# Kernel optimization log

Measured on AMD Instinct MI355X. Metric: run time of the kernel, lower is better.

The kernel has to match this reference:

```python
import jax, jax.numpy as jnp
import numpy as np

N_NODES = 50000
N_EDGES = 800000
N_GRAPHS = 64
IN_C, HID_C, OUT_C = 768, 128, 1


def setup_inputs() -> dict:
    key = jax.random.key(0)
    ks = jax.random.split(key, 9)
    x = jax.random.normal(ks[0], (N_NODES, IN_C), dtype=jnp.float32)
    edge_index = jax.random.randint(ks[1], (2, N_EDGES), 0, N_NODES, dtype=jnp.int32)
    batch = jnp.sort(jax.random.randint(ks[2], (N_NODES,), 0, N_GRAPHS, dtype=jnp.int32))
    s1 = 1.0 / np.sqrt(IN_C)
    s2 = 1.0 / np.sqrt(HID_C)
    W1 = jax.random.normal(ks[3], (IN_C, HID_C), dtype=jnp.float32) * s1
    b1 = jnp.zeros((HID_C,), dtype=jnp.float32)
    W2 = jax.random.normal(ks[4], (HID_C, HID_C), dtype=jnp.float32) * s2
    b2 = jnp.zeros((HID_C,), dtype=jnp.float32)
    Wl = jax.random.normal(ks[5], (HID_C, OUT_C), dtype=jnp.float32) * s2
    bl = jnp.zeros((OUT_C,), dtype=jnp.float32)
    return {"x": x, "edge_index": edge_index, "batch": batch,
            "W1": W1, "b1": b1, "W2": W2, "b2": b2, "Wl": Wl, "bl": bl}


def gcn_conv(x, W, b, src, dst, n_nodes):
    """PyG GCNConv: linear transform, symmetric norm with self-loops, scatter-add."""
    xl = x @ W  # [N, C_out]
    # in-degree including self-loop
    deg = jax.ops.segment_sum(jnp.ones_like(dst, dtype=xl.dtype), dst,
                              num_segments=n_nodes) + 1.0
    dinv = jax.lax.rsqrt(deg)  # deg >= 1 so safe
    norm = dinv[src] * dinv[dst]  # [E]
    agg = jax.ops.segment_sum(norm[:, None] * xl[src], dst, num_segments=n_nodes)
    # self-loop message: dinv[i]^2 * xl[i]
    agg = agg + xl * (dinv * dinv)[:, None]
    return agg + b


def reference(x, edge_index, batch, W1, b1, W2, b2, Wl, bl):
    src, dst = edge_index[0], edge_index[1]
    n = x.shape[0]
    h = jax.nn.relu(gcn_conv(x, W1, b1, src, dst, n))
    # dropout is identity in eval mode
    h = jax.nn.relu(gcn_conv(h, W2, b2, src, dst, n))
    # global mean pool over graphs
    sums = jax.ops.segment_sum(h, batch, num_segments=N_GRAPHS)
    cnts = jax.ops.segment_sum(jnp.ones((n,), dtype=h.dtype), batch,
                               num_segments=N_GRAPHS)
    pooled = sums / jnp.maximum(cnts, 1.0)[:, None]
    return pooled @ Wl + bl
```

## Files before the change

kernel.cpp:

```cpp
#include <hip/hip_runtime.h>

#define N_NODES  50000
#define N_EDGES  800000
#define N_GRAPHS 64
#define N_CHUNK  4
#define ZREP     16
#define SCAN_BLOCKS 196
#define GATHER_BLOCKS 1568

typedef unsigned short u16x8 __attribute__((ext_vector_type(8)));
typedef short s16x8 __attribute__((ext_vector_type(8)));
typedef float f32x4 __attribute__((ext_vector_type(4)));

__device__ __forceinline__ float bf2f(unsigned short h) {
    return __uint_as_float((unsigned)h << 16);
}
__device__ __forceinline__ unsigned short f2bf(float f) {
    unsigned u = __float_as_uint(f);
    unsigned r = (u + 0x7FFFu + ((u >> 16) & 1u)) >> 16;
    return (unsigned short)r;
}
__device__ __forceinline__ unsigned pk2(float a, float b) {
    return (unsigned)f2bf(a) | ((unsigned)f2bf(b) << 16);
}


__global__ void zero_int_kernel(int* __restrict__ p, int n) {
    for (int i = blockIdx.x * blockDim.x + threadIdx.x; i < n; i += gridDim.x * blockDim.x)
        p[i] = 0;
}

__global__ void hist_kernel(const int* __restrict__ ei, int* __restrict__ cnt) {
    const int* dst = ei + N_EDGES;
    for (int e = blockIdx.x * blockDim.x + threadIdx.x; e < N_EDGES; e += gridDim.x * blockDim.x)
        atomicAdd(&cnt[dst[e]], 1);
}

__global__ void scanA_kernel(const int* __restrict__ cnt, int* __restrict__ bsum,
                             float* __restrict__ dinv) {
    __shared__ int wsum[4];
    int t = threadIdx.x;
    int i = blockIdx.x * 256 + t;
    int v = cnt[i];
    if (i < N_NODES) dinv[i] = rsqrtf((float)v + 1.f);
    int s = v;
    #pragma unroll
    for (int off = 1; off < 64; off <<= 1) s += __shfl_xor(s, off);
    if ((t & 63) == 0) wsum[t >> 6] = s;
    __syncthreads();
    if (t == 0) bsum[blockIdx.x] = wsum[0] + wsum[1] + wsum[2] + wsum[3];
}

__global__ void scanB_kernel(const int* __restrict__ bsum, int* __restrict__ boff) {
    __shared__ int wsum[4];
    int t = threadIdx.x;
    int lane = t & 63, w = t >> 6;
    int v = (t < SCAN_BLOCKS) ? bsum[t] : 0;
    int s = v;
    #pragma unroll
    for (int off = 1; off < 64; off <<= 1) {
        int u = __shfl_up(s, off);
        if (lane >= off) s += u;
    }
    if (lane == 63) wsum[w] = s;
    __syncthreads();
    int wo = 0;
    for (int j = 0; j < w; ++j) wo += wsum[j];
    if (t < SCAN_BLOCKS) boff[t] = wo + s - v;
}

__global__ void scanC_kernel(int* __restrict__ cnt, const int* __restrict__ boff,
                             int* __restrict__ rowptr) {
    __shared__ int wsum[4];
    int t = threadIdx.x;
    int i = blockIdx.x * 256 + t;
    int lane = t & 63, w = t >> 6;
    int v = cnt[i];
    int s = v;
    #pragma unroll
    for (int off = 1; off < 64; off <<= 1) {
        int u = __shfl_up(s, off);
        if (lane >= off) s += u;
    }
    if (lane == 63) wsum[w] = s;
    __syncthreads();
    int wo = 0;
    for (int j = 0; j < w; ++j) wo += wsum[j];
    rowptr[i] = boff[blockIdx.x] + wo + s - v;
    cnt[i] = 0;
}

__global__ void fill_kernel(const int* __restrict__ ei, const int* __restrict__ rowptr,
                            int* __restrict__ fill, const float* __restrict__ dinv,
                            int2* __restrict__ csr) {
    const int* src = ei;
    const int* dst = ei + N_EDGES;
    for (int e = blockIdx.x * blockDim.x + threadIdx.x; e < N_EDGES; e += gridDim.x * blockDim.x) {
        int s = src[e], d = dst[e];
        int pos = rowptr[d] + atomicAdd(&fill[d], 1);
        csr[pos] = make_int2(s, __float_as_int(dinv[s] * dinv[d]));
    }
}

__global__ void gcount_bs_kernel(const int* __restrict__ batch, float* __restrict__ cntg,
                                 float* __restrict__ zsumR) {
    int g = threadIdx.x;
    if (g >= N_GRAPHS) return;
    #pragma unroll
    for (int r = 0; r < ZREP; ++r) zsumR[r * N_GRAPHS + g] = 0.f;
    int lo = 0, hi = N_NODES;
    while (lo < hi) { int mid = (lo + hi) >> 1; if (batch[mid] < g) lo = mid + 1; else hi = mid; }
    int a = lo;
    lo = 0; hi = N_NODES;
    while (lo < hi) { int mid = (lo + hi) >> 1; if (batch[mid] < g + 1) lo = mid + 1; else hi = mid; }
    cntg[g] = (float)(lo - a);
}

__global__ void prep_w_kernel(const float* __restrict__ W1, const float* __restrict__ W2,
                              unsigned short* __restrict__ w1h, unsigned short* __restrict__ w1l,
                              unsigned short* __restrict__ w2h, unsigned short* __restrict__ w2l) {
    const int n1 = 768 * 128, n2 = 128 * 128;
    for (int i = blockIdx.x * blockDim.x + threadIdx.x; i < n1 + n2; i += gridDim.x * blockDim.x) {
        if (i < n1) {
            int k = i >> 7, c = i & 127;
            float w = W1[i];
            unsigned short hi = f2bf(w);
            unsigned short lo = f2bf(w - bf2f(hi));
            w1h[c * 768 + k] = hi;
            w1l[c * 768 + k] = lo;
        } else {
            int j = i - n1;
            int k = j >> 7, c = j & 127;
            float w = W2[j];
            unsigned short hi = f2bf(w);
            unsigned short lo = f2bf(w - bf2f(hi));
            w2h[c * 128 + k] = hi;
            w2l[c * 128 + k] = lo;
        }
    }
}

template<int K, bool BF16A>
__global__ __launch_bounds__(256) void gemm_mfma(const void* __restrict__ Av,
                                                 const unsigned short* __restrict__ Wth,
                                                 const unsigned short* __restrict__ Wtl,
                                                 unsigned short* __restrict__ C, int M) {
    __shared__ unsigned short Xs[128 * 40];
    __shared__ unsigned short Wh[128 * 40];
    __shared__ unsigned short Wl[128 * 40];

    const int tid  = threadIdx.x;
    const int row0 = blockIdx.x * 128;
    const int trow  = tid >> 1;
    const int thalf = (tid & 1) * 16;

    int grow = row0 + trow;
    if (grow >= M) grow = M - 1;
    const float* xpf = (const float*)Av + (long)grow * K + thalf;
    const unsigned short* xpb = (const unsigned short*)Av + (long)grow * K + thalf;
    const unsigned short* wph = Wth + (long)trow * K + thalf;
    const unsigned short* wpl = Wtl + (long)trow * K + thalf;

    f32x4 acc[8][2];
    #pragma unroll
    for (int rf = 0; rf < 8; ++rf)
        #pragma unroll
        for (int cf = 0; cf < 2; ++cf)
            acc[rf][cf] = (f32x4){0.f, 0.f, 0.f, 0.f};

    float4 f0, f1, f2, f3;
    uint4 b0, b1;
    if constexpr (!BF16A) {
        f0 = *(const float4*)(xpf);
        f1 = *(const float4*)(xpf + 4);
        f2 = *(const float4*)(xpf + 8);
        f3 = *(const float4*)(xpf + 12);
    } else {
        b0 = *(const uint4*)(xpb);
        b1 = *(const uint4*)(xpb + 8);
    }

    const int l   = tid & 63;
    const int wv  = tid >> 6;
    const int lr  = l & 15;
    const int lk8 = (l >> 4) * 8;

    for (int k0 = 0; k0 < K; k0 += 32) {
        uint4 wh0 = ((const uint4*)(wph + k0))[0];
        uint4 wh1 = ((const uint4*)(wph + k0))[1];
        uint4 wl0 = ((const uint4*)(wpl + k0))[0];
        uint4 wl1 = ((const uint4*)(wpl + k0))[1];
        unsigned short* xrow = &Xs[trow * 40 + thalf];
        if constexpr (!BF16A) {
            *(uint4*)(xrow)     = make_uint4(pk2(f0.x, f0.y), pk2(f0.z, f0.w), pk2(f1.x, f1.y), pk2(f1.z, f1.w));
            *(uint4*)(xrow + 8) = make_uint4(pk2(f2.x, f2.y), pk2(f2.z, f2.w), pk2(f3.x, f3.y), pk2(f3.z, f3.w));
        } else {
            *(uint4*)(xrow)     = b0;
            *(uint4*)(xrow + 8) = b1;
        }
        *(uint4*)&Wh[trow * 40 + thalf]     = wh0;
        *(uint4*)&Wh[trow * 40 + thalf + 8] = wh1;
        *(uint4*)&Wl[trow * 40 + thalf]     = wl0;
        *(uint4*)&Wl[trow * 40 + thalf + 8] = wl1;
        __syncthreads();

        if (k0 + 32 < K) {
            if constexpr (!BF16A) {
                f0 = *(const float4*)(xpf + k0 + 32);
                f1 = *(const float4*)(xpf + k0 + 36);
                f2 = *(const float4*)(xpf + k0 + 40);
                f3 = *(const float4*)(xpf + k0 + 44);
            } else {
                b0 = *(const uint4*)(xpb + k0 + 32);
                b1 = *(const uint4*)(xpb + k0 + 40);
            }
        }

        s16x8 xb[8], whf[2], wlf[2];
        #pragma unroll
        for (int rf = 0; rf < 8; ++rf)
            xb[rf] = *(const s16x8*)&Xs[(rf * 16 + lr) * 40 + lk8];
        #pragma unroll
        for (int cf = 0; cf < 2; ++cf) {
            whf[cf] = *(const s16x8*)&Wh[(wv * 32 + cf * 16 + lr) * 40 + lk8];
            wlf[cf] = *(const s16x8*)&Wl[(wv * 32 + cf * 16 + lr) * 40 + lk8];
        }
        #pragma unroll
        for (int rf = 0; rf < 8; ++rf)
            #pragma unroll
            for (int cf = 0; cf < 2; ++cf) {
                acc[rf][cf] = __builtin_amdgcn_mfma_f32_16x16x32_bf16(wlf[cf], xb[rf], acc[rf][cf], 0, 0, 0);
                acc[rf][cf] = __builtin_amdgcn_mfma_f32_16x16x32_bf16(whf[cf], xb[rf], acc[rf][cf], 0, 0, 0);
            }
        __syncthreads();
    }

    const int c4 = (l >> 4) * 4;
    #pragma unroll
    for (int rf = 0; rf < 8; ++rf) {
        int r = row0 + rf * 16 + lr;
        if (r < M) {
            #pragma unroll
            for (int cf = 0; cf < 2; ++cf) {
                int cb = wv * 32 + cf * 16 + c4;
                ushort4 v;
                v.x = f2bf(acc[rf][cf][0]);
                v.y = f2bf(acc[rf][cf][1]);
                v.z = f2bf(acc[rf][cf][2]);
                v.w = f2bf(acc[rf][cf][3]);
                *(ushort4*)(C + ((long)(cb >> 5) * N_NODES + r) * 32 + (cb & 31)) = v;
            }
        }
    }
}

template<int MODE>
__global__ __launch_bounds__(256, 6) void gather_all_kernel(
        const unsigned short* __restrict__ xlc, const float* __restrict__ dinv,
        const int* __restrict__ rowptr, const int2* __restrict__ csr,
        const float* __restrict__ bias, unsigned short* __restrict__ outbuf,
        const float* __restrict__ Wl, const int* __restrict__ batch,
        float* __restrict__ zsumR) {
    const int lane = threadIdx.x & 63;
    const int half = lane & 1;
    const int c0   = half * 16;

    const int grp   = blockIdx.x & 7;
    const int chunk = grp & 3;
    const unsigned short* xc = xlc + (long)chunk * N_NODES * 32;

    const int cblk = (blockIdx.x >> 3) + (grp >> 2) * 196;
    const int wvc  = cblk * 4 + (threadIdx.x >> 6);
    const int slot = wvc * 32 + (lane >> 1);
    const bool vn  = slot < N_NODES;
    const int node = vn ? slot : N_NODES - 1;

    const int start = rowptr[node];
    const int end   = vn ? rowptr[node + 1] : start;
    const float di  = dinv[node];

    const u16x8* srow = (const u16x8*)(xc + (long)node * 32 + c0);
    u16x8 s0 = srow[0], s1 = srow[1];

    float acc[16];
    #pragma unroll
    for (int j = 0; j < 16; ++j) acc[j] = 0.f;

    int e = start;
    for (; e + 1 < end; e += 2) {
        int2 cA = csr[e];
        int2 cB = csr[e + 1];
        float wA = __int_as_float(cA.y);
        float wB = __int_as_float(cB.y);
        const u16x8* rA = (const u16x8*)(xc + (long)cA.x * 32 + c0);
        const u16x8* rB = (const u16x8*)(xc + (long)cB.x * 32 + c0);
        u16x8 a0 = rA[0], a1 = rA[1];
        u16x8 b0 = rB[0], b1 = rB[1];
        #pragma unroll
        for (int j = 0; j < 8; ++j) {
            acc[j]     = fmaf(wA, bf2f(a0[j]), acc[j]);
            acc[j + 8] = fmaf(wA, bf2f(a1[j]), acc[j + 8]);
        }
        #pragma unroll
        for (int j = 0; j < 8; ++j) {
            acc[j]     = fmaf(wB, bf2f(b0[j]), acc[j]);
            acc[j + 8] = fmaf(wB, bf2f(b1[j]), acc[j + 8]);
        }
    }
    if (e < end) {
        int2 cA = csr[e];
        float wA = __int_as_float(cA.y);
        const u16x8* rA = (const u16x8*)(xc + (long)cA.x * 32 + c0);
        u16x8 a0 = rA[0], a1 = rA[1];
        #pragma unroll
        for (int j = 0; j < 8; ++j) {
            acc[j]     = fmaf(wA, bf2f(a0[j]), acc[j]);
            acc[j + 8] = fmaf(wA, bf2f(a1[j]), acc[j + 8]);
        }
    }

    const float w2 = di * di;
    const float* bch = bias + chunk * 32 + c0;
    float s[16];
    #pragma unroll
    for (int j = 0; j < 8; ++j) {
        s[j]     = fmaxf(fmaf(w2, bf2f(s0[j]), acc[j])     + bch[j],     0.f);
        s[j + 8] = fmaxf(fmaf(w2, bf2f(s1[j]), acc[j + 8]) + bch[j + 8], 0.f);
    }

    if (MODE == 0) {
        if (vn) {
            unsigned short* op = outbuf + (long)node * 128 + chunk * 32 + c0;
            u16x8 o0, o1;
            #pragma unroll
            for (int j = 0; j < 8; ++j) {
                o0[j] = f2bf(s[j]);
                o1[j] = f2bf(s[j + 8]);
            }
            ((u16x8*)op)[0] = o0;
            ((u16x8*)op)[1] = o1;
        }
    } else {
        const float* wch = Wl + chunk * 32 + c0;
        float z = 0.f;
        #pragma unroll
        for (int j = 0; j < 16; ++j) z = fmaf(s[j], wch[j], z);
        z += __shfl_xor(z, 1);
        if (!vn || half) z = 0.f;
        int b = batch[node];
        int b0v = __shfl(b, 0);
        bool uniform = __all(b == b0v);
        if (uniform) {
            #pragma unroll
            for (int off = 1; off < 64; off <<= 1) z += __shfl_xor(z, off);
            if (lane == 0)
                atomicAdd(&zsumR[(blockIdx.x & (ZREP - 1)) * N_GRAPHS + b0v], z);
        } else if (vn && !half) {
            atomicAdd(&zsumR[((lane >> 1) & (ZREP - 1)) * N_GRAPHS + b], z);
        }
    }
}

__global__ void out_kernel(const float* __restrict__ zsumR, const float* __restrict__ cntg,
                           const float* __restrict__ bl, float* __restrict__ out) {
    int g = threadIdx.x;
    if (g < N_GRAPHS) {
        float z = 0.f;
        #pragma unroll
        for (int r = 0; r < ZREP; ++r) z += zsumR[r * N_GRAPHS + g];
        out[g] = z / fmaxf(cntg[g], 1.f) + bl[0];
    }
}


extern "C" void kernel_launch(void* const* d_in, const int* in_sizes, int n_in,
                              void* d_out, int out_size, void* d_ws, size_t ws_size,
                              hipStream_t stream) {
    const float* x    = (const float*)d_in[0];
    const int*   ei   = (const int*)d_in[1];
    const int*   batch= (const int*)d_in[2];
    const float* W1   = (const float*)d_in[3];
    const float* b1   = (const float*)d_in[4];
    const float* W2   = (const float*)d_in[5];
    const float* b2   = (const float*)d_in[6];
    const float* Wl   = (const float*)d_in[7];
    const float* bl   = (const float*)d_in[8];
    float* out = (float*)d_out;

    float* ws      = (float*)d_ws;
    float* dinv    = ws;
    float* zsumR   = ws + 50176;
    float* cntg    = ws + 51200;
    int*   cnt_i   = (int*)(ws + 51264);
    int*   rowptr  = (int*)(ws + 101440);
    int2*  csr     = (int2*)(ws + 151616);
    unsigned short* xl16 = (unsigned short*)(ws + 1751616);
    unsigned short* h1   = (unsigned short*)(ws + 1751616 + 3200000);
    unsigned short* w1h = (unsigned short*)(ws + 11351616);
    unsigned short* w1l = w1h + 98304;
    unsigned short* w2h = w1l + 98304;
    unsigned short* w2l = w2h + 16384;
    int* bsum = (int*)(w2l + 16384);
    int* boff = bsum + 256;

    zero_int_kernel<<<128, 256, 0, stream>>>(cnt_i, 50176);

    hist_kernel<<<1024, 256, 0, stream>>>(ei, cnt_i);
    scanA_kernel<<<SCAN_BLOCKS, 256, 0, stream>>>(cnt_i, bsum, dinv);
    scanB_kernel<<<1, 256, 0, stream>>>(bsum, boff);
    scanC_kernel<<<SCAN_BLOCKS, 256, 0, stream>>>(cnt_i, boff, rowptr);
    fill_kernel<<<1024, 256, 0, stream>>>(ei, rowptr, cnt_i, dinv, csr);
    gcount_bs_kernel<<<1, 64, 0, stream>>>(batch, cntg, zsumR);
    prep_w_kernel<<<448, 256, 0, stream>>>(W1, W2, w1h, w1l, w2h, w2l);

    gemm_mfma<768, false><<<391, 256, 0, stream>>>(x, w1h, w1l, xl16, N_NODES);
    gather_all_kernel<0><<<GATHER_BLOCKS, 256, 0, stream>>>(
        xl16, dinv, rowptr, csr, b1, h1, nullptr, nullptr, nullptr);

    gemm_mfma<128, true><<<391, 256, 0, stream>>>(h1, w2h, w2l, xl16, N_NODES);
    gather_all_kernel<1><<<GATHER_BLOCKS, 256, 0, stream>>>(
        xl16, dinv, rowptr, csr, b2, nullptr, Wl, batch, zsumR);

    out_kernel<<<1, 64, 0, stream>>>(zsumR, cntg, bl, out);
}
```

Before: 246.9 us.

## Halve GEMM row tile, prefetch weights, unroll gather by four, fuse graph-count kernel

The GEMM row tile shrinks from 128 to 64 rows per block, which doubles the grid to 782 blocks so more CUs stay busy, and weight tiles are now prefetched into registers one k-step ahead. The edge gather loop is unrolled from two to four edges so more independent loads are in flight. The per-graph count and zero-init work moves into the single-block scanB kernel, removing one launch. The smaller tile means each weight tile is reused across fewer rows, so weight traffic per output goes up.

```diff
diff --git a/kernel.cpp b/kernel.cpp
--- a/kernel.cpp
+++ b/kernel.cpp
@@ -51,7 +51,9 @@
     if (t == 0) bsum[blockIdx.x] = wsum[0] + wsum[1] + wsum[2] + wsum[3];
 }
 
-__global__ void scanB_kernel(const int* __restrict__ bsum, int* __restrict__ boff) {
+__global__ void scanB_kernel(const int* __restrict__ bsum, int* __restrict__ boff,
+                             const int* __restrict__ batch, float* __restrict__ cntg,
+                             float* __restrict__ zsumR) {
     __shared__ int wsum[4];
     int t = threadIdx.x;
     int lane = t & 63, w = t >> 6;
@@ -67,6 +69,18 @@
     int wo = 0;
     for (int j = 0; j < w; ++j) wo += wsum[j];
     if (t < SCAN_BLOCKS) boff[t] = wo + s - v;
+
+    if (t < N_GRAPHS) {
+        #pragma unroll
+        for (int r = 0; r < ZREP; ++r) zsumR[r * N_GRAPHS + t] = 0.f;
+        int g = t;
+        int lo = 0, hi = N_NODES;
+        while (lo < hi) { int mid = (lo + hi) >> 1; if (batch[mid] < g) lo = mid + 1; else hi = mid; }
+        int a = lo;
+        lo = 0; hi = N_NODES;
+        while (lo < hi) { int mid = (lo + hi) >> 1; if (batch[mid] < g + 1) lo = mid + 1; else hi = mid; }
+        cntg[g] = (float)(lo - a);
+    }
 }
 
 __global__ void scanC_kernel(int* __restrict__ cnt, const int* __restrict__ boff,
@@ -100,20 +114,6 @@
         int pos = rowptr[d] + atomicAdd(&fill[d], 1);
         csr[pos] = make_int2(s, __float_as_int(dinv[s] * dinv[d]));
     }
-}
-
-__global__ void gcount_bs_kernel(const int* __restrict__ batch, float* __restrict__ cntg,
-                                 float* __restrict__ zsumR) {
-    int g = threadIdx.x;
-    if (g >= N_GRAPHS) return;
-    #pragma unroll
-    for (int r = 0; r < ZREP; ++r) zsumR[r * N_GRAPHS + g] = 0.f;
-    int lo = 0, hi = N_NODES;
-    while (lo < hi) { int mid = (lo + hi) >> 1; if (batch[mid] < g) lo = mid + 1; else hi = mid; }
-    int a = lo;
-    lo = 0; hi = N_NODES;
-    while (lo < hi) { int mid = (lo + hi) >> 1; if (batch[mid] < g + 1) lo = mid + 1; else hi = mid; }
-    cntg[g] = (float)(lo - a);
 }
 
 __global__ void prep_w_kernel(const float* __restrict__ W1, const float* __restrict__ W2,
@@ -145,40 +145,44 @@
                                                  const unsigned short* __restrict__ Wth,
                                                  const unsigned short* __restrict__ Wtl,
                                                  unsigned short* __restrict__ C, int M) {
-    __shared__ unsigned short Xs[128 * 40];
+    __shared__ unsigned short Xs[64 * 40];
     __shared__ unsigned short Wh[128 * 40];
     __shared__ unsigned short Wl[128 * 40];
 
     const int tid  = threadIdx.x;
-    const int row0 = blockIdx.x * 128;
-    const int trow  = tid >> 1;
-    const int thalf = (tid & 1) * 16;
-
-    int grow = row0 + trow;
+    const int row0 = blockIdx.x * 64;
+
+    const int xr = tid >> 2;
+    const int xq = (tid & 3) * 8;
+    int grow = row0 + xr;
     if (grow >= M) grow = M - 1;
-    const float* xpf = (const float*)Av + (long)grow * K + thalf;
-    const unsigned short* xpb = (const unsigned short*)Av + (long)grow * K + thalf;
-    const unsigned short* wph = Wth + (long)trow * K + thalf;
-    const unsigned short* wpl = Wtl + (long)trow * K + thalf;
-
-    f32x4 acc[8][2];
-    #pragma unroll
-    for (int rf = 0; rf < 8; ++rf)
+    const float* xpf = (const float*)Av + (long)grow * K + xq;
+    const unsigned short* xpb = (const unsigned short*)Av + (long)grow * K + xq;
+
+    const int wc = tid >> 1;
+    const int wh16 = (tid & 1) * 16;
+    const unsigned short* wph = Wth + (long)wc * K + wh16;
+    const unsigned short* wpl = Wtl + (long)wc * K + wh16;
+
+    f32x4 acc[4][2];
+    #pragma unroll
+    for (int rf = 0; rf < 4; ++rf)
         #pragma unroll
         for (int cf = 0; cf < 2; ++cf)
             acc[rf][cf] = (f32x4){0.f, 0.f, 0.f, 0.f};
 
-    float4 f0, f1, f2, f3;
-    uint4 b0, b1;
+    float4 f0, f1;
+    uint4 xr0;
     if constexpr (!BF16A) {
         f0 = *(const float4*)(xpf);
         f1 = *(const float4*)(xpf + 4);
-        f2 = *(const float4*)(xpf + 8);
-        f3 = *(const float4*)(xpf + 12);
     } else {
-        b0 = *(const uint4*)(xpb);
-        b1 = *(const uint4*)(xpb + 8);
-    }
+        xr0 = *(const uint4*)(xpb);
+    }
+    uint4 whr0 = *(const uint4*)(wph);
+    uint4 whr1 = *(const uint4*)(wph + 8);
+    uint4 wlr0 = *(const uint4*)(wpl);
+    uint4 wlr1 = *(const uint4*)(wpl + 8);
 
     const int l   = tid & 63;
     const int wv  = tid >> 6;
@@ -186,39 +190,33 @@
     const int lk8 = (l >> 4) * 8;
 
     for (int k0 = 0; k0 < K; k0 += 32) {
-        uint4 wh0 = ((const uint4*)(wph + k0))[0];
-        uint4 wh1 = ((const uint4*)(wph + k0))[1];
-        uint4 wl0 = ((const uint4*)(wpl + k0))[0];
-        uint4 wl1 = ((const uint4*)(wpl + k0))[1];
-        unsigned short* xrow = &Xs[trow * 40 + thalf];
-        if constexpr (!BF16A) {
-            *(uint4*)(xrow)     = make_uint4(pk2(f0.x, f0.y), pk2(f0.z, f0.w), pk2(f1.x, f1.y), pk2(f1.z, f1.w));
-            *(uint4*)(xrow + 8) = make_uint4(pk2(f2.x, f2.y), pk2(f2.z, f2.w), pk2(f3.x, f3.y), pk2(f3.z, f3.w));
-        } else {
-            *(uint4*)(xrow)     = b0;
-            *(uint4*)(xrow + 8) = b1;
-        }
-        *(uint4*)&Wh[trow * 40 + thalf]     = wh0;
-        *(uint4*)&Wh[trow * 40 + thalf + 8] = wh1;
-        *(uint4*)&Wl[trow * 40 + thalf]     = wl0;
-        *(uint4*)&Wl[trow * 40 + thalf + 8] = wl1;
+        if constexpr (!BF16A)
+            *(uint4*)&Xs[xr * 40 + xq] = make_uint4(pk2(f0.x, f0.y), pk2(f0.z, f0.w),
+                                                    pk2(f1.x, f1.y), pk2(f1.z, f1.w));
+        else
+            *(uint4*)&Xs[xr * 40 + xq] = xr0;
+        *(uint4*)&Wh[wc * 40 + wh16]     = whr0;
+        *(uint4*)&Wh[wc * 40 + wh16 + 8] = whr1;
+        *(uint4*)&Wl[wc * 40 + wh16]     = wlr0;
+        *(uint4*)&Wl[wc * 40 + wh16 + 8] = wlr1;
         __syncthreads();
 
         if (k0 + 32 < K) {
             if constexpr (!BF16A) {
                 f0 = *(const float4*)(xpf + k0 + 32);
                 f1 = *(const float4*)(xpf + k0 + 36);
-                f2 = *(const float4*)(xpf + k0 + 40);
-                f3 = *(const float4*)(xpf + k0 + 44);
             } else {
-                b0 = *(const uint4*)(xpb + k0 + 32);
-                b1 = *(const uint4*)(xpb + k0 + 40);
+                xr0 = *(const uint4*)(xpb + k0 + 32);
             }
-        }
-
-        s16x8 xb[8], whf[2], wlf[2];
-        #pragma unroll
-        for (int rf = 0; rf < 8; ++rf)
+            whr0 = *(const uint4*)(wph + k0 + 32);
+            whr1 = *(const uint4*)(wph + k0 + 40);
+            wlr0 = *(const uint4*)(wpl + k0 + 32);
+            wlr1 = *(const uint4*)(wpl + k0 + 40);
+        }
+
+        s16x8 xb[4], whf[2], wlf[2];
+        #pragma unroll
+        for (int rf = 0; rf < 4; ++rf)
             xb[rf] = *(const s16x8*)&Xs[(rf * 16 + lr) * 40 + lk8];
         #pragma unroll
         for (int cf = 0; cf < 2; ++cf) {
@@ -226,7 +224,7 @@
             wlf[cf] = *(const s16x8*)&Wl[(wv * 32 + cf * 16 + lr) * 40 + lk8];
         }
         #pragma unroll
-        for (int rf = 0; rf < 8; ++rf)
+        for (int rf = 0; rf < 4; ++rf)
             #pragma unroll
             for (int cf = 0; cf < 2; ++cf) {
                 acc[rf][cf] = __builtin_amdgcn_mfma_f32_16x16x32_bf16(wlf[cf], xb[rf], acc[rf][cf], 0, 0, 0);
@@ -237,7 +235,7 @@
 
     const int c4 = (l >> 4) * 4;
     #pragma unroll
-    for (int rf = 0; rf < 8; ++rf) {
+    for (int rf = 0; rf < 4; ++rf) {
         int r = row0 + rf * 16 + lr;
         if (r < M) {
             #pragma unroll
@@ -287,15 +285,23 @@
     for (int j = 0; j < 16; ++j) acc[j] = 0.f;
 
     int e = start;
-    for (; e + 1 < end; e += 2) {
+    for (; e + 3 < end; e += 4) {
         int2 cA = csr[e];
         int2 cB = csr[e + 1];
+        int2 cC = csr[e + 2];
+        int2 cD = csr[e + 3];
         float wA = __int_as_float(cA.y);
         float wB = __int_as_float(cB.y);
+        float wC = __int_as_float(cC.y);
+        float wD = __int_as_float(cD.y);
         const u16x8* rA = (const u16x8*)(xc + (long)cA.x * 32 + c0);
         const u16x8* rB = (const u16x8*)(xc + (long)cB.x * 32 + c0);
+        const u16x8* rC = (const u16x8*)(xc + (long)cC.x * 32 + c0);
+        const u16x8* rD = (const u16x8*)(xc + (long)cD.x * 32 + c0);
         u16x8 a0 = rA[0], a1 = rA[1];
         u16x8 b0 = rB[0], b1 = rB[1];
+        u16x8 d0 = rC[0], d1 = rC[1];
+        u16x8 e0 = rD[0], e1 = rD[1];
         #pragma unroll
         for (int j = 0; j < 8; ++j) {
             acc[j]     = fmaf(wA, bf2f(a0[j]), acc[j]);
@@ -306,8 +312,18 @@
             acc[j]     = fmaf(wB, bf2f(b0[j]), acc[j]);
             acc[j + 8] = fmaf(wB, bf2f(b1[j]), acc[j + 8]);
         }
-    }
-    if (e < end) {
+        #pragma unroll
+        for (int j = 0; j < 8; ++j) {
+            acc[j]     = fmaf(wC, bf2f(d0[j]), acc[j]);
+            acc[j + 8] = fmaf(wC, bf2f(d1[j]), acc[j + 8]);
+        }
+        #pragma unroll
+        for (int j = 0; j < 8; ++j) {
+            acc[j]     = fmaf(wD, bf2f(e0[j]), acc[j]);
+            acc[j + 8] = fmaf(wD, bf2f(e1[j]), acc[j + 8]);
+        }
+    }
+    for (; e < end; ++e) {
         int2 cA = csr[e];
         float wA = __int_as_float(cA.y);
         const u16x8* rA = (const u16x8*)(xc + (long)cA.x * 32 + c0);
@@ -407,17 +423,16 @@
 
     hist_kernel<<<1024, 256, 0, stream>>>(ei, cnt_i);
     scanA_kernel<<<SCAN_BLOCKS, 256, 0, stream>>>(cnt_i, bsum, dinv);
-    scanB_kernel<<<1, 256, 0, stream>>>(bsum, boff);
+    scanB_kernel<<<1, 256, 0, stream>>>(bsum, boff, batch, cntg, zsumR);
     scanC_kernel<<<SCAN_BLOCKS, 256, 0, stream>>>(cnt_i, boff, rowptr);
     fill_kernel<<<1024, 256, 0, stream>>>(ei, rowptr, cnt_i, dinv, csr);
-    gcount_bs_kernel<<<1, 64, 0, stream>>>(batch, cntg, zsumR);
     prep_w_kernel<<<448, 256, 0, stream>>>(W1, W2, w1h, w1l, w2h, w2l);
 
-    gemm_mfma<768, false><<<391, 256, 0, stream>>>(x, w1h, w1l, xl16, N_NODES);
+    gemm_mfma<768, false><<<782, 256, 0, stream>>>(x, w1h, w1l, xl16, N_NODES);
     gather_all_kernel<0><<<GATHER_BLOCKS, 256, 0, stream>>>(
         xl16, dinv, rowptr, csr, b1, h1, nullptr, nullptr, nullptr);
 
-    gemm_mfma<128, true><<<391, 256, 0, stream>>>(h1, w2h, w2l, xl16, N_NODES);
+    gemm_mfma<128, true><<<782, 256, 0, stream>>>(h1, w2h, w2l, xl16, N_NODES);
     gather_all_kernel<1><<<GATHER_BLOCKS, 256, 0, stream>>>(
         xl16, dinv, rowptr, csr, b2, nullptr, Wl, batch, zsumR);
 
```

New measurement: 249.1 us. No clear change (+0.9%).

## Fuse graph-count kernel into scan, prefetch GEMM weights, unroll gather by four

Applied to the files above, without the earlier changes.

Folds the per-graph node count and pooled-sum zeroing into the single-block scanB kernel, removing one kernel launch. In the MFMA GEMM, the weight hi/lo tiles for the next K step are now loaded into registers during the current step, like the activations already were, so global latency overlaps compute. The gather loop is unrolled to four edges per iteration with a scalar remainder loop, putting more independent row loads in flight at the cost of higher register pressure.

```diff
diff --git a/kernel.cpp b/kernel.cpp
--- a/kernel.cpp
+++ b/kernel.cpp
@@ -51,7 +51,9 @@
     if (t == 0) bsum[blockIdx.x] = wsum[0] + wsum[1] + wsum[2] + wsum[3];
 }
 
-__global__ void scanB_kernel(const int* __restrict__ bsum, int* __restrict__ boff) {
+__global__ void scanB_kernel(const int* __restrict__ bsum, int* __restrict__ boff,
+                             const int* __restrict__ batch, float* __restrict__ cntg,
+                             float* __restrict__ zsumR) {
     __shared__ int wsum[4];
     int t = threadIdx.x;
     int lane = t & 63, w = t >> 6;
@@ -67,6 +69,18 @@
     int wo = 0;
     for (int j = 0; j < w; ++j) wo += wsum[j];
     if (t < SCAN_BLOCKS) boff[t] = wo + s - v;
+
+    if (t < N_GRAPHS) {
+        #pragma unroll
+        for (int r = 0; r < ZREP; ++r) zsumR[r * N_GRAPHS + t] = 0.f;
+        int g = t;
+        int lo = 0, hi = N_NODES;
+        while (lo < hi) { int mid = (lo + hi) >> 1; if (batch[mid] < g) lo = mid + 1; else hi = mid; }
+        int a = lo;
+        lo = 0; hi = N_NODES;
+        while (lo < hi) { int mid = (lo + hi) >> 1; if (batch[mid] < g + 1) lo = mid + 1; else hi = mid; }
+        cntg[g] = (float)(lo - a);
+    }
 }
 
 __global__ void scanC_kernel(int* __restrict__ cnt, const int* __restrict__ boff,
@@ -100,20 +114,6 @@
         int pos = rowptr[d] + atomicAdd(&fill[d], 1);
         csr[pos] = make_int2(s, __float_as_int(dinv[s] * dinv[d]));
     }
-}
-
-__global__ void gcount_bs_kernel(const int* __restrict__ batch, float* __restrict__ cntg,
-                                 float* __restrict__ zsumR) {
-    int g = threadIdx.x;
-    if (g >= N_GRAPHS) return;
-    #pragma unroll
-    for (int r = 0; r < ZREP; ++r) zsumR[r * N_GRAPHS + g] = 0.f;
-    int lo = 0, hi = N_NODES;
-    while (lo < hi) { int mid = (lo + hi) >> 1; if (batch[mid] < g) lo = mid + 1; else hi = mid; }
-    int a = lo;
-    lo = 0; hi = N_NODES;
-    while (lo < hi) { int mid = (lo + hi) >> 1; if (batch[mid] < g + 1) lo = mid + 1; else hi = mid; }
-    cntg[g] = (float)(lo - a);
 }
 
 __global__ void prep_w_kernel(const float* __restrict__ W1, const float* __restrict__ W2,
@@ -169,16 +169,20 @@
             acc[rf][cf] = (f32x4){0.f, 0.f, 0.f, 0.f};
 
     float4 f0, f1, f2, f3;
-    uint4 b0, b1;
+    uint4 xb0, xb1;
     if constexpr (!BF16A) {
         f0 = *(const float4*)(xpf);
         f1 = *(const float4*)(xpf + 4);
         f2 = *(const float4*)(xpf + 8);
         f3 = *(const float4*)(xpf + 12);
     } else {
-        b0 = *(const uint4*)(xpb);
-        b1 = *(const uint4*)(xpb + 8);
-    }
+        xb0 = *(const uint4*)(xpb);
+        xb1 = *(const uint4*)(xpb + 8);
+    }
+    uint4 wh0 = ((const uint4*)(wph))[0];
+    uint4 wh1 = ((const uint4*)(wph))[1];
+    uint4 wl0 = ((const uint4*)(wpl))[0];
+    uint4 wl1 = ((const uint4*)(wpl))[1];
 
     const int l   = tid & 63;
     const int wv  = tid >> 6;
@@ -186,17 +190,13 @@
     const int lk8 = (l >> 4) * 8;
 
     for (int k0 = 0; k0 < K; k0 += 32) {
-        uint4 wh0 = ((const uint4*)(wph + k0))[0];
-        uint4 wh1 = ((const uint4*)(wph + k0))[1];
-        uint4 wl0 = ((const uint4*)(wpl + k0))[0];
-        uint4 wl1 = ((const uint4*)(wpl + k0))[1];
         unsigned short* xrow = &Xs[trow * 40 + thalf];
         if constexpr (!BF16A) {
             *(uint4*)(xrow)     = make_uint4(pk2(f0.x, f0.y), pk2(f0.z, f0.w), pk2(f1.x, f1.y), pk2(f1.z, f1.w));
             *(uint4*)(xrow + 8) = make_uint4(pk2(f2.x, f2.y), pk2(f2.z, f2.w), pk2(f3.x, f3.y), pk2(f3.z, f3.w));
         } else {
-            *(uint4*)(xrow)     = b0;
-            *(uint4*)(xrow + 8) = b1;
+            *(uint4*)(xrow)     = xb0;
+            *(uint4*)(xrow + 8) = xb1;
         }
         *(uint4*)&Wh[trow * 40 + thalf]     = wh0;
         *(uint4*)&Wh[trow * 40 + thalf + 8] = wh1;
@@ -211,9 +211,13 @@
                 f2 = *(const float4*)(xpf + k0 + 40);
                 f3 = *(const float4*)(xpf + k0 + 44);
             } else {
-                b0 = *(const uint4*)(xpb + k0 + 32);
-                b1 = *(const uint4*)(xpb + k0 + 40);
+                xb0 = *(const uint4*)(xpb + k0 + 32);
+                xb1 = *(const uint4*)(xpb + k0 + 40);
             }
+            wh0 = ((const uint4*)(wph + k0 + 32))[0];
+            wh1 = ((const uint4*)(wph + k0 + 32))[1];
+            wl0 = ((const uint4*)(wpl + k0 + 32))[0];
+            wl1 = ((const uint4*)(wpl + k0 + 32))[1];
         }
 
         s16x8 xb[8], whf[2], wlf[2];
@@ -287,15 +291,23 @@
     for (int j = 0; j < 16; ++j) acc[j] = 0.f;
 
     int e = start;
-    for (; e + 1 < end; e += 2) {
+    for (; e + 3 < end; e += 4) {
         int2 cA = csr[e];
         int2 cB = csr[e + 1];
+        int2 cC = csr[e + 2];
+        int2 cD = csr[e + 3];
         float wA = __int_as_float(cA.y);
         float wB = __int_as_float(cB.y);
+        float wC = __int_as_float(cC.y);
+        float wD = __int_as_float(cD.y);
         const u16x8* rA = (const u16x8*)(xc + (long)cA.x * 32 + c0);
         const u16x8* rB = (const u16x8*)(xc + (long)cB.x * 32 + c0);
+        const u16x8* rC = (const u16x8*)(xc + (long)cC.x * 32 + c0);
+        const u16x8* rD = (const u16x8*)(xc + (long)cD.x * 32 + c0);
         u16x8 a0 = rA[0], a1 = rA[1];
         u16x8 b0 = rB[0], b1 = rB[1];
+        u16x8 d0 = rC[0], d1 = rC[1];
+        u16x8 e0 = rD[0], e1 = rD[1];
         #pragma unroll
         for (int j = 0; j < 8; ++j) {
             acc[j]     = fmaf(wA, bf2f(a0[j]), acc[j]);
@@ -306,8 +318,18 @@
             acc[j]     = fmaf(wB, bf2f(b0[j]), acc[j]);
             acc[j + 8] = fmaf(wB, bf2f(b1[j]), acc[j + 8]);
         }
-    }
-    if (e < end) {
+        #pragma unroll
+        for (int j = 0; j < 8; ++j) {
+            acc[j]     = fmaf(wC, bf2f(d0[j]), acc[j]);
+            acc[j + 8] = fmaf(wC, bf2f(d1[j]), acc[j + 8]);
+        }
+        #pragma unroll
+        for (int j = 0; j < 8; ++j) {
+            acc[j]     = fmaf(wD, bf2f(e0[j]), acc[j]);
+            acc[j + 8] = fmaf(wD, bf2f(e1[j]), acc[j + 8]);
+        }
+    }
+    for (; e < end; ++e) {
         int2 cA = csr[e];
         float wA = __int_as_float(cA.y);
         const u16x8* rA = (const u16x8*)(xc + (long)cA.x * 32 + c0);
@@ -407,10 +429,9 @@
 
     hist_kernel<<<1024, 256, 0, stream>>>(ei, cnt_i);
     scanA_kernel<<<SCAN_BLOCKS, 256, 0, stream>>>(cnt_i, bsum, dinv);
-    scanB_kernel<<<1, 256, 0, stream>>>(bsum, boff);
+    scanB_kernel<<<1, 256, 0, stream>>>(bsum, boff, batch, cntg, zsumR);
     scanC_kernel<<<SCAN_BLOCKS, 256, 0, stream>>>(cnt_i, boff, rowptr);
     fill_kernel<<<1024, 256, 0, stream>>>(ei, rowptr, cnt_i, dinv, csr);
-    gcount_bs_kernel<<<1, 64, 0, stream>>>(batch, cntg, zsumR);
     prep_w_kernel<<<448, 256, 0, stream>>>(W1, W2, w1h, w1l, w2h, w2l);
 
     gemm_mfma<768, false><<<391, 256, 0, stream>>>(x, w1h, w1l, xl16, N_NODES);
```

Result: faster. 236.5 us (-4.2%).
